# Performance work log

Measured on AMD Instinct MI355X. Metric: run time of the kernel, lower is better.

The kernel has to match this reference:

```python
import jax, jax.numpy as jnp
import numpy as np

B, S, D = 4, 2048, 1024
H = 16
HD = D // H  # 64


def setup_inputs() -> dict:
    key = jax.random.key(0)
    ks = jax.random.split(key, 4)
    scale = 0.02
    return {
        "hidden_states": jax.random.normal(ks[0], (B, S, D), dtype=jnp.float32),
        "attention_mask": jnp.zeros((B, 1, 1, S), dtype=jnp.float32),
        "Wq": jax.random.normal(ks[1], (D, D), dtype=jnp.float32) * scale,
        "bq": jnp.zeros((D,), dtype=jnp.float32),
        "Wk": jax.random.normal(ks[2], (D, D), dtype=jnp.float32) * scale,
        "bk": jnp.zeros((D,), dtype=jnp.float32),
        "Wv": jax.random.normal(ks[3], (D, D), dtype=jnp.float32) * scale,
        "bv": jnp.zeros((D,), dtype=jnp.float32),
    }


def reference(hidden_states, attention_mask, Wq, bq, Wk, bk, Wv, bv):
    # linear projections: x @ W^T + b (torch nn.Linear convention); here W stored as [D,D]
    def proj(x, W, b):
        y = jnp.einsum("bsd,ed->bse", x, W) + b
        # [B,S,D] -> [B,H,S,HD]
        return y.reshape(B, S, H, HD).transpose(0, 2, 1, 3)

    q = proj(hidden_states, Wq, bq)
    k = proj(hidden_states, Wk, bk)
    v = proj(hidden_states, Wv, bv)

    scores = jnp.einsum("bhqd,bhkd->bhqk", q, k) / jnp.sqrt(jnp.float32(HD))
    scores = scores + attention_mask  # additive mask broadcast [B,1,1,S]
    probs = jax.nn.softmax(scores, axis=-1)  # dropout p=0 -> identity
    ctx = jnp.einsum("bhqk,bhkd->bhqd", probs, v)
    ctx = ctx.transpose(0, 2, 1, 3).reshape(B, S, D)
    return ctx
```

## Files before the change

### kernel.cpp

```cpp
#include <hip/hip_runtime.h>
#include <hip/hip_bf16.h>

typedef __attribute__((ext_vector_type(4))) float f32x4;
typedef __attribute__((ext_vector_type(16))) float f32x16;
typedef __attribute__((ext_vector_type(8))) short bf16x8;
typedef __attribute__((ext_vector_type(4))) unsigned int u32x4;
typedef unsigned short u16;

#define DEV static __device__ __forceinline__

DEV u16 f2bf(float f) {
    union { float f; unsigned int u; } v; v.f = f;
    unsigned int r = v.u + 0x7FFFu + ((v.u >> 16) & 1u);
    return (u16)(r >> 16);
}

DEV unsigned int cvt_pk(float lo, float hi) {
    unsigned int r;
    asm("v_cvt_pk_bf16_f32 %0, %1, %2" : "=v"(r) : "v"(lo), "v"(hi));
    return r;
}

DEV void pswap(unsigned int& a, unsigned int& b) {
    asm volatile("v_permlane32_swap_b32 %0, %1" : "+v"(a), "+v"(b));
}

DEV void async16(const void* g, void* l) {
    __builtin_amdgcn_global_load_lds((const __attribute__((address_space(1))) unsigned int*)g,
                                     (__attribute__((address_space(3))) unsigned int*)l, 16, 0, 0);
}

__global__ void cvt_all(const float4* __restrict__ x, const float4* __restrict__ wq,
                        const float4* __restrict__ wk, const float4* __restrict__ wv,
                        ushort4* __restrict__ xb, ushort4* __restrict__ wb,
                        const float* __restrict__ mask, float* __restrict__ em) {
    int bid = blockIdx.x;
    if (bid >= 11264) {
        int i = (bid - 11264) * 256 + threadIdx.x;
        em[i] = __builtin_amdgcn_exp2f(mask[i] * 1.44269504088896340736f);
        return;
    }
    const float4* s;
    ushort4* d;
    int i;
    if (bid < 8192) {
        s = x; d = xb; i = bid * 256 + threadIdx.x;
    } else {
        int r = bid - 8192;
        int wsel = r >> 10;
        s = (wsel == 0) ? wq : (wsel == 1) ? wk : wv;
        d = wb + (size_t)wsel * 262144;
        i = (r & 1023) * 256 + threadIdx.x;
    }
    float4 v = s[i];
    ushort4 o;
    o.x = f2bf(v.x); o.y = f2bf(v.y); o.z = f2bf(v.z); o.w = f2bf(v.w);
    d[i] = o;
}

__launch_bounds__(256, 2)
__global__ void qkv_gemm(const u16* __restrict__ xb, const u16* __restrict__ wb,
                         const float* __restrict__ bq, const float* __restrict__ bk,
                         const float* __restrict__ bv, const float* __restrict__ em,
                         u16* __restrict__ Qb, u16* __restrict__ Kb, u16* __restrict__ Vtb) {
    __shared__ u16 Al[2][128 * 64];
    __shared__ u16 Bl[2][128 * 64];
    const int t = threadIdx.x, ln = t & 63, w = t >> 6;
    const int wr = w >> 1, wc = w & 1;
    const int m0 = blockIdx.x * 128, e0 = blockIdx.y * 128, p = blockIdx.z;
    const u16* Wp = wb + (size_t)p * 1048576;
    const float* bias = (p == 0) ? bq : (p == 1) ? bk : bv;

    const int srow = t >> 3, scol = (t & 7) * 8;

    f32x4 acc[4][4];
#pragma unroll
    for (int i = 0; i < 4; i++)
#pragma unroll
        for (int j = 0; j < 4; j++) acc[i][j] = (f32x4){0.f, 0.f, 0.f, 0.f};

#define G_STAGE(buf, kk)                                                              \
    {                                                                                 \
        _Pragma("unroll")                                                             \
        for (int c = 0; c < 4; c++) {                                                 \
            int r = c * 32 + srow;                                                    \
            async16(&xb[(size_t)(m0 + r) * 1024 + (kk) + scol], &Al[buf][r * 64 + scol]); \
            async16(&Wp[(size_t)(e0 + r) * 1024 + (kk) + scol], &Bl[buf][r * 64 + scol]); \
        }                                                                             \
    }

    G_STAGE(0, 0);
    __syncthreads();
    int cur = 0;
    for (int kt = 0; kt < 16; kt++) {
        if (kt < 15) G_STAGE(cur ^ 1, (kt + 1) * 64);
#pragma unroll
        for (int kc = 0; kc < 2; kc++) {
            bf16x8 a[4], bb[4];
#pragma unroll
            for (int mf = 0; mf < 4; mf++)
                a[mf] = *(const bf16x8*)&Al[cur][(wr * 64 + mf * 16 + (ln & 15)) * 64 + kc * 32 + (ln >> 4) * 8];
#pragma unroll
            for (int nf = 0; nf < 4; nf++)
                bb[nf] = *(const bf16x8*)&Bl[cur][(wc * 64 + nf * 16 + (ln & 15)) * 64 + kc * 32 + (ln >> 4) * 8];
            __builtin_amdgcn_s_setprio(1);
#pragma unroll
            for (int mf = 0; mf < 4; mf++)
#pragma unroll
                for (int nf = 0; nf < 4; nf++)
                    acc[mf][nf] = __builtin_amdgcn_mfma_f32_16x16x32_bf16(a[mf], bb[nf], acc[mf][nf], 0, 0, 0);
            __builtin_amdgcn_s_setprio(0);
        }
        __syncthreads();
        cur ^= 1;
    }
#undef G_STAGE

    const int q16 = ln & 15, g = ln >> 4;
    if (p == 2) {
#pragma unroll
        for (int nf = 0; nf < 4; nf++) {
            int e = e0 + wc * 64 + nf * 16 + q16;
            float bias_v = bias[e];
            int h = e >> 6, hd = e & 63;
#pragma unroll
            for (int mf = 0; mf < 4; mf++) {
                int m = m0 + wr * 64 + mf * 16 + g * 4;
                int b = m >> 11, s = m & 2047;
                f32x4 emv = *(const f32x4*)&em[b * 2048 + s];
                ushort4 pk;
                pk.x = f2bf((acc[mf][nf][0] + bias_v) * emv[0]);
                pk.y = f2bf((acc[mf][nf][1] + bias_v) * emv[1]);
                pk.z = f2bf((acc[mf][nf][2] + bias_v) * emv[2]);
                pk.w = f2bf((acc[mf][nf][3] + bias_v) * emv[3]);
                *(ushort4*)&Vtb[((size_t)((b * 16 + h) * 64 + hd)) * 2048 + s] = pk;
            }
        }
    } else {
        const float qscale = (p == 0) ? 0.18033688011112042f : 1.0f;
        u16* out = (p == 0) ? Qb : Kb;
#pragma unroll
        for (int nf = 0; nf < 4; nf++) {
            int e = e0 + wc * 64 + nf * 16 + q16;
            float bias_v = bias[e];
            int h = e >> 6, hd = e & 63;
#pragma unroll
            for (int mf = 0; mf < 4; mf++) {
#pragma unroll
                for (int r = 0; r < 4; r++) {
                    int m = m0 + wr * 64 + mf * 16 + g * 4 + r;
                    int b = m >> 11, s = m & 2047;
                    out[((size_t)(b * 16 + h) * 2048 + s) * 64 + hd] = f2bf((acc[mf][nf][r] + bias_v) * qscale);
                }
            }
        }
    }
}

__launch_bounds__(128, 2)
__global__ void attn_kernel(const u16* __restrict__ Q, const u16* __restrict__ K,
                            const u16* __restrict__ Vt, const float* __restrict__ em,
                            float* __restrict__ out) {
    __shared__ u16 Kl[2][64 * 64];
    __shared__ u16 Vl[2][64 * 64];
    const int t = threadIdx.x, ln = t & 63, w = t >> 6;
    const int ln31 = ln & 31, hi = ln >> 5, ln7 = ln & 7;

    const int bid0 = blockIdx.x;
    const int swz = (bid0 & 7) * 128 + (bid0 >> 3);
    const int qbi = swz & 15, bh = swz >> 4;
    const int b = bh >> 4, h = bh & 15;
    const int qr = qbi * 128 + w * 64;
    const size_t base = (size_t)bh * 2048 * 64;

    bf16x8 aq[2][4];
#pragma unroll
    for (int qt = 0; qt < 2; qt++)
#pragma unroll
        for (int ds = 0; ds < 4; ds++)
            aq[qt][ds] = *(const bf16x8*)&Q[base + (size_t)(qr + qt * 32 + ln31) * 64 + ds * 16 + hi * 8];

    const int rbase = t >> 3;
    const int sc = (t & 7) ^ (rbase & 7);

#define A_STAGE(buf, kk)                                                                   \
    {                                                                                      \
        _Pragma("unroll")                                                                  \
        for (int i = 0; i < 4; i++) {                                                      \
            int row = i * 16 + rbase;                                                      \
            async16(&K[base + (size_t)((kk) + row) * 64 + sc * 8], &Kl[buf][(i * 128 + t) * 8]); \
            async16(&Vt[base + (size_t)row * 2048 + (kk) + sc * 8], &Vl[buf][(i * 128 + t) * 8]); \
        }                                                                                  \
    }

    f32x16 accT[2][2];
    f32x4 lacc[2];
#pragma unroll
    for (int dt = 0; dt < 2; dt++)
#pragma unroll
        for (int qt = 0; qt < 2; qt++) accT[dt][qt] = (f32x16){};
    lacc[0] = (f32x4){0.f, 0.f, 0.f, 0.f};
    lacc[1] = (f32x4){0.f, 0.f, 0.f, 0.f};

    A_STAGE(0, 0);
    __syncthreads();
    int cur = 0;

    for (int kt = 0; kt < 32; kt++) {
        const int k0 = kt * 64;
        if (kt < 31) A_STAGE(cur ^ 1, k0 + 64);

#pragma unroll
        for (int kti = 0; kti < 2; kti++) {
            bf16x8 ka[4];
#pragma unroll
            for (int ds = 0; ds < 4; ds++)
                ka[ds] = *(const bf16x8*)&Kl[cur][(kti * 32 + ln31) * 64 + (((ds << 1) | hi) ^ ln7) * 8];

            f32x4 em4[4];
#pragma unroll
            for (int rf = 0; rf < 4; rf++)
                em4[rf] = *(const f32x4*)&em[b * 2048 + k0 + kti * 32 + rf * 8 + hi * 4];

            u32x4 pb[2][2];
#pragma unroll
            for (int qt = 0; qt < 2; qt++) {
                f32x16 z = (f32x16){};
                __builtin_amdgcn_s_setprio(1);
#pragma unroll
                for (int ds = 0; ds < 4; ds++)
                    z = __builtin_amdgcn_mfma_f32_32x32x16_bf16(ka[ds], aq[qt][ds], z, 0, 0, 0);
                __builtin_amdgcn_s_setprio(0);

                float p[16];
#pragma unroll
                for (int i = 0; i < 16; i++) p[i] = __builtin_amdgcn_exp2f(z[i]);

#pragma unroll
                for (int rf = 0; rf < 4; rf++) {
                    lacc[qt][0] += p[4 * rf + 0] * em4[rf][0];
                    lacc[qt][1] += p[4 * rf + 1] * em4[rf][1];
                    lacc[qt][2] += p[4 * rf + 2] * em4[rf][2];
                    lacc[qt][3] += p[4 * rf + 3] * em4[rf][3];
                }

                unsigned int pk00 = cvt_pk(p[0], p[1]),  pk01 = cvt_pk(p[2], p[3]);
                unsigned int pk10 = cvt_pk(p[4], p[5]),  pk11 = cvt_pk(p[6], p[7]);
                unsigned int pk20 = cvt_pk(p[8], p[9]),  pk21 = cvt_pk(p[10], p[11]);
                unsigned int pk30 = cvt_pk(p[12], p[13]), pk31 = cvt_pk(p[14], p[15]);
                pswap(pk00, pk10); pswap(pk01, pk11);
                pswap(pk20, pk30); pswap(pk21, pk31);
                pb[qt][0][0] = pk00; pb[qt][0][1] = pk01; pb[qt][0][2] = pk10; pb[qt][0][3] = pk11;
                pb[qt][1][0] = pk20; pb[qt][1][1] = pk21; pb[qt][1][2] = pk30; pb[qt][1][3] = pk31;
            }

            __builtin_amdgcn_s_setprio(1);
#pragma unroll
            for (int s = 0; s < 2; s++) {
#pragma unroll
                for (int dt = 0; dt < 2; dt++) {
                    bf16x8 va = *(const bf16x8*)&Vl[cur][(dt * 32 + ln31) * 64 +
                                                         ((kti * 4 + s * 2 + hi) ^ ln7) * 8];
#pragma unroll
                    for (int qt = 0; qt < 2; qt++) {
                        bf16x8 pv = *(const bf16x8*)&pb[qt][s];
                        accT[dt][qt] = __builtin_amdgcn_mfma_f32_32x32x16_bf16(va, pv, accT[dt][qt], 0, 0, 0);
                    }
                }
            }
            __builtin_amdgcn_s_setprio(0);
        }

        __syncthreads();
        cur ^= 1;
    }
#undef A_STAGE

#pragma unroll
    for (int qt = 0; qt < 2; qt++) {
        float l = (lacc[qt][0] + lacc[qt][1]) + (lacc[qt][2] + lacc[qt][3]);
        l += __shfl_xor(l, 32);
        float inv = 1.0f / l;
        int q = qr + qt * 32 + ln31;
#pragma unroll
        for (int dt = 0; dt < 2; dt++) {
#pragma unroll
            for (int rf = 0; rf < 4; rf++) {
                f32x4 o;
                o[0] = accT[dt][qt][4 * rf + 0] * inv;
                o[1] = accT[dt][qt][4 * rf + 1] * inv;
                o[2] = accT[dt][qt][4 * rf + 2] * inv;
                o[3] = accT[dt][qt][4 * rf + 3] * inv;
                *(f32x4*)&out[((size_t)(b * 2048 + q)) * 1024 + h * 64 + dt * 32 + rf * 8 + hi * 4] = o;
            }
        }
    }
}

extern "C" void kernel_launch(void* const* d_in, const int* in_sizes, int n_in,
                              void* d_out, int out_size, void* d_ws, size_t ws_size,
                              hipStream_t stream) {
    const float* x    = (const float*)d_in[0];
    const float* mask = (const float*)d_in[1];
    const float* Wq   = (const float*)d_in[2];
    const float* bq   = (const float*)d_in[3];
    const float* Wk   = (const float*)d_in[4];
    const float* bk   = (const float*)d_in[5];
    const float* Wv   = (const float*)d_in[6];
    const float* bv   = (const float*)d_in[7];
    float* out = (float*)d_out;

    char* ws = (char*)d_ws;
    if (ws_size < (size_t)73433088) return;
    u16* xb   = (u16*)(ws);
    u16* wb   = (u16*)(ws + 16777216);
    u16* Qb   = (u16*)(ws + 23068672);
    u16* Kb   = (u16*)(ws + 39845888);
    u16* Vtb  = (u16*)(ws + 56623104);
    float* em = (float*)(ws + 73400320);

    cvt_all<<<11296, 256, 0, stream>>>((const float4*)x, (const float4*)Wq, (const float4*)Wk,
                                       (const float4*)Wv, (ushort4*)xb, (ushort4*)wb, mask, em);
    qkv_gemm<<<dim3(64, 8, 3), 256, 0, stream>>>(xb, wb, bq, bk, bv, em, Qb, Kb, Vtb);
    attn_kernel<<<1024, 128, 0, stream>>>(Qb, Kb, Vtb, em, out);
}
```

Measured before the change: 172.7 us.

## Halve attention query tile per block and drop LDS double buffering

Each wave now handles 32 query rows instead of 64, so the grid doubles to 2048 blocks. The K/V shared-memory staging goes from double buffering to a single buffer, with a sync before and after each load. Launch bounds rise to 3 blocks per CU to gain occupancy from fewer registers and less LDS. The cost is that each K/V tile loaded from global memory is reused by half as many queries, and async loads no longer overlap compute within a block.

After: 196.5 us. 13.8% more time.

```diff
diff --git a/kernel.cpp b/kernel.cpp
--- a/kernel.cpp
+++ b/kernel.cpp
@@ -157,142 +157,122 @@
     }
 }
 
-__launch_bounds__(128, 2)
+__launch_bounds__(128, 3)
 __global__ void attn_kernel(const u16* __restrict__ Q, const u16* __restrict__ K,
                             const u16* __restrict__ Vt, const float* __restrict__ em,
                             float* __restrict__ out) {
-    __shared__ u16 Kl[2][64 * 64];
-    __shared__ u16 Vl[2][64 * 64];
+    __shared__ u16 Kl[64 * 64];
+    __shared__ u16 Vl[64 * 64];
     const int t = threadIdx.x, ln = t & 63, w = t >> 6;
     const int ln31 = ln & 31, hi = ln >> 5, ln7 = ln & 7;
 
     const int bid0 = blockIdx.x;
-    const int swz = (bid0 & 7) * 128 + (bid0 >> 3);
-    const int qbi = swz & 15, bh = swz >> 4;
+    const int swz = (bid0 & 7) * 256 + (bid0 >> 3);
+    const int qbi = swz & 31, bh = swz >> 5;
     const int b = bh >> 4, h = bh & 15;
-    const int qr = qbi * 128 + w * 64;
+    const int qr = qbi * 64 + w * 32;
     const size_t base = (size_t)bh * 2048 * 64;
 
-    bf16x8 aq[2][4];
-#pragma unroll
-    for (int qt = 0; qt < 2; qt++)
-#pragma unroll
-        for (int ds = 0; ds < 4; ds++)
-            aq[qt][ds] = *(const bf16x8*)&Q[base + (size_t)(qr + qt * 32 + ln31) * 64 + ds * 16 + hi * 8];
+    bf16x8 aq[4];
+#pragma unroll
+    for (int ds = 0; ds < 4; ds++)
+        aq[ds] = *(const bf16x8*)&Q[base + (size_t)(qr + ln31) * 64 + ds * 16 + hi * 8];
 
     const int rbase = t >> 3;
     const int sc = (t & 7) ^ (rbase & 7);
 
-#define A_STAGE(buf, kk)                                                                   \
+#define A_STAGE(kk)                                                                        \
     {                                                                                      \
         _Pragma("unroll")                                                                  \
         for (int i = 0; i < 4; i++) {                                                      \
             int row = i * 16 + rbase;                                                      \
-            async16(&K[base + (size_t)((kk) + row) * 64 + sc * 8], &Kl[buf][(i * 128 + t) * 8]); \
-            async16(&Vt[base + (size_t)row * 2048 + (kk) + sc * 8], &Vl[buf][(i * 128 + t) * 8]); \
+            async16(&K[base + (size_t)((kk) + row) * 64 + sc * 8], &Kl[(i * 128 + t) * 8]); \
+            async16(&Vt[base + (size_t)row * 2048 + (kk) + sc * 8], &Vl[(i * 128 + t) * 8]); \
         }                                                                                  \
     }
 
-    f32x16 accT[2][2];
-    f32x4 lacc[2];
-#pragma unroll
-    for (int dt = 0; dt < 2; dt++)
-#pragma unroll
-        for (int qt = 0; qt < 2; qt++) accT[dt][qt] = (f32x16){};
-    lacc[0] = (f32x4){0.f, 0.f, 0.f, 0.f};
-    lacc[1] = (f32x4){0.f, 0.f, 0.f, 0.f};
-
-    A_STAGE(0, 0);
-    __syncthreads();
-    int cur = 0;
+    f32x16 accT[2];
+    accT[0] = (f32x16){};
+    accT[1] = (f32x16){};
+    f32x4 lacc = (f32x4){0.f, 0.f, 0.f, 0.f};
 
     for (int kt = 0; kt < 32; kt++) {
         const int k0 = kt * 64;
-        if (kt < 31) A_STAGE(cur ^ 1, k0 + 64);
+        if (kt) __syncthreads();
+        A_STAGE(k0);
+        __syncthreads();
 
 #pragma unroll
         for (int kti = 0; kti < 2; kti++) {
             bf16x8 ka[4];
 #pragma unroll
             for (int ds = 0; ds < 4; ds++)
-                ka[ds] = *(const bf16x8*)&Kl[cur][(kti * 32 + ln31) * 64 + (((ds << 1) | hi) ^ ln7) * 8];
+                ka[ds] = *(const bf16x8*)&Kl[(kti * 32 + ln31) * 64 + (((ds << 1) | hi) ^ ln7) * 8];
 
             f32x4 em4[4];
 #pragma unroll
             for (int rf = 0; rf < 4; rf++)
                 em4[rf] = *(const f32x4*)&em[b * 2048 + k0 + kti * 32 + rf * 8 + hi * 4];
 
-            u32x4 pb[2][2];
-#pragma unroll
-            for (int qt = 0; qt < 2; qt++) {
-                f32x16 z = (f32x16){};
-                __builtin_amdgcn_s_setprio(1);
-#pragma unroll
-                for (int ds = 0; ds < 4; ds++)
-                    z = __builtin_amdgcn_mfma_f32_32x32x16_bf16(ka[ds], aq[qt][ds], z, 0, 0, 0);
-                __builtin_amdgcn_s_setprio(0);
-
-                float p[16];
-#pragma unroll
-                for (int i = 0; i < 16; i++) p[i] = __builtin_amdgcn_exp2f(z[i]);
-
-#pragma unroll
-                for (int rf = 0; rf < 4; rf++) {
-                    lacc[qt][0] += p[4 * rf + 0] * em4[rf][0];
-                    lacc[qt][1] += p[4 * rf + 1] * em4[rf][1];
-                    lacc[qt][2] += p[4 * rf + 2] * em4[rf][2];
-                    lacc[qt][3] += p[4 * rf + 3] * em4[rf][3];
-                }
-
-                unsigned int pk00 = cvt_pk(p[0], p[1]),  pk01 = cvt_pk(p[2], p[3]);
-                unsigned int pk10 = cvt_pk(p[4], p[5]),  pk11 = cvt_pk(p[6], p[7]);
-                unsigned int pk20 = cvt_pk(p[8], p[9]),  pk21 = cvt_pk(p[10], p[11]);
-                unsigned int pk30 = cvt_pk(p[12], p[13]), pk31 = cvt_pk(p[14], p[15]);
-                pswap(pk00, pk10); pswap(pk01, pk11);
-                pswap(pk20, pk30); pswap(pk21, pk31);
-                pb[qt][0][0] = pk00; pb[qt][0][1] = pk01; pb[qt][0][2] = pk10; pb[qt][0][3] = pk11;
-                pb[qt][1][0] = pk20; pb[qt][1][1] = pk21; pb[qt][1][2] = pk30; pb[qt][1][3] = pk31;
+            f32x16 z = (f32x16){};
+            __builtin_amdgcn_s_setprio(1);
+#pragma unroll
+            for (int ds = 0; ds < 4; ds++)
+                z = __builtin_amdgcn_mfma_f32_32x32x16_bf16(ka[ds], aq[ds], z, 0, 0, 0);
+            __builtin_amdgcn_s_setprio(0);
+
+            float p[16];
+#pragma unroll
+            for (int i = 0; i < 16; i++) p[i] = __builtin_amdgcn_exp2f(z[i]);
+
+#pragma unroll
+            for (int rf = 0; rf < 4; rf++) {
+                lacc[0] += p[4 * rf + 0] * em4[rf][0];
+                lacc[1] += p[4 * rf + 1] * em4[rf][1];
+                lacc[2] += p[4 * rf + 2] * em4[rf][2];
+                lacc[3] += p[4 * rf + 3] * em4[rf][3];
             }
 
+            unsigned int pk00 = cvt_pk(p[0], p[1]),   pk01 = cvt_pk(p[2], p[3]);
+            unsigned int pk10 = cvt_pk(p[4], p[5]),   pk11 = cvt_pk(p[6], p[7]);
+            unsigned int pk20 = cvt_pk(p[8], p[9]),   pk21 = cvt_pk(p[10], p[11]);
+            unsigned int pk30 = cvt_pk(p[12], p[13]), pk31 = cvt_pk(p[14], p[15]);
+            pswap(pk00, pk10); pswap(pk01, pk11);
+            pswap(pk20, pk30); pswap(pk21, pk31);
+            u32x4 pb[2];
+            pb[0][0] = pk00; pb[0][1] = pk01; pb[0][2] = pk10; pb[0][3] = pk11;
+            pb[1][0] = pk20; pb[1][1] = pk21; pb[1][2] = pk30; pb[1][3] = pk31;
+
             __builtin_amdgcn_s_setprio(1);
 #pragma unroll
             for (int s = 0; s < 2; s++) {
+                bf16x8 pv = *(const bf16x8*)&pb[s];
 #pragma unroll
                 for (int dt = 0; dt < 2; dt++) {
-                    bf16x8 va = *(const bf16x8*)&Vl[cur][(dt * 32 + ln31) * 64 +
-                                                         ((kti * 4 + s * 2 + hi) ^ ln7) * 8];
-#pragma unroll
-                    for (int qt = 0; qt < 2; qt++) {
-                        bf16x8 pv = *(const bf16x8*)&pb[qt][s];
-                        accT[dt][qt] = __builtin_amdgcn_mfma_f32_32x32x16_bf16(va, pv, accT[dt][qt], 0, 0, 0);
-                    }
+                    bf16x8 va = *(const bf16x8*)&Vl[(dt * 32 + ln31) * 64 +
+                                                    ((kti * 4 + s * 2 + hi) ^ ln7) * 8];
+                    accT[dt] = __builtin_amdgcn_mfma_f32_32x32x16_bf16(va, pv, accT[dt], 0, 0, 0);
                 }
             }
             __builtin_amdgcn_s_setprio(0);
         }
-
-        __syncthreads();
-        cur ^= 1;
     }
 #undef A_STAGE
 
-#pragma unroll
-    for (int qt = 0; qt < 2; qt++) {
-        float l = (lacc[qt][0] + lacc[qt][1]) + (lacc[qt][2] + lacc[qt][3]);
-        l += __shfl_xor(l, 32);
-        float inv = 1.0f / l;
-        int q = qr + qt * 32 + ln31;
-#pragma unroll
-        for (int dt = 0; dt < 2; dt++) {
-#pragma unroll
-            for (int rf = 0; rf < 4; rf++) {
-                f32x4 o;
-                o[0] = accT[dt][qt][4 * rf + 0] * inv;
-                o[1] = accT[dt][qt][4 * rf + 1] * inv;
-                o[2] = accT[dt][qt][4 * rf + 2] * inv;
-                o[3] = accT[dt][qt][4 * rf + 3] * inv;
-                *(f32x4*)&out[((size_t)(b * 2048 + q)) * 1024 + h * 64 + dt * 32 + rf * 8 + hi * 4] = o;
-            }
+    float l = (lacc[0] + lacc[1]) + (lacc[2] + lacc[3]);
+    l += __shfl_xor(l, 32);
+    float inv = 1.0f / l;
+    int q = qr + ln31;
+#pragma unroll
+    for (int dt = 0; dt < 2; dt++) {
+#pragma unroll
+        for (int rf = 0; rf < 4; rf++) {
+            f32x4 o;
+            o[0] = accT[dt][4 * rf + 0] * inv;
+            o[1] = accT[dt][4 * rf + 1] * inv;
+            o[2] = accT[dt][4 * rf + 2] * inv;
+            o[3] = accT[dt][4 * rf + 3] * inv;
+            *(f32x4*)&out[((size_t)(b * 2048 + q)) * 1024 + h * 64 + dt * 32 + rf * 8 + hi * 4] = o;
         }
     }
 }
@@ -322,5 +302,5 @@
     cvt_all<<<11296, 256, 0, stream>>>((const float4*)x, (const float4*)Wq, (const float4*)Wk,
                                        (const float4*)Wv, (ushort4*)xb, (ushort4*)wb, mask, em);
     qkv_gemm<<<dim3(64, 8, 3), 256, 0, stream>>>(xb, wb, bq, bk, bv, em, Qb, Kb, Vtb);
-    attn_kernel<<<1024, 128, 0, stream>>>(Qb, Kb, Vtb, em, out);
-}
+    attn_kernel<<<2048, 128, 0, stream>>>(Qb, Kb, Vtb, em, out);
+}
```
